# Kernel tuning notes

Measured on AMD Instinct MI355X. Metric: run time of the kernel, lower is better.

## Reference

```python
import jax, jax.numpy as jnp
import numpy as np

N_NODES = 200000
AVG_DEG = 64
N_EDGES = N_NODES * AVG_DEG
ALPHA = 0.1
DT = 0.01
EPS = 1e-9
DIFF = 10.0
HARD_LO = -jnp.pi / 2
HARD_HI = jnp.pi / 2


def setup_inputs() -> dict:
    key = jax.random.key(0)
    ks = jax.random.split(key, 8)
    xy = jax.random.normal(ks[0], (N_NODES, 2), dtype=jnp.float32)
    xy_dot_old = jax.random.normal(ks[1], (N_NODES, 2), dtype=jnp.float32)
    scale = 2.0 * np.pi
    phase = (jax.random.uniform(ks[2], (N_NODES,), dtype=jnp.float32) * 2 - 1) * scale
    w = (jax.random.uniform(ks[3], (N_NODES,), dtype=jnp.float32) * 2 - 1) * scale
    amplitudes = (jax.random.uniform(ks[4], (N_NODES,), dtype=jnp.float32) * 2 - 1) * scale
    ha = jax.random.normal(ks[5], (N_NODES,), dtype=jnp.float32)
    edge_src = jnp.sort(jax.random.randint(ks[6], (N_EDGES,), 0, N_NODES, dtype=jnp.int32))
    edge_dst = jax.random.randint(ks[7], (N_EDGES,), 0, N_NODES, dtype=jnp.int32)
    return {
        "xy": xy,
        "xy_dot_old": xy_dot_old,
        "phase": phase,
        "w": w,
        "amplitudes": amplitudes,
        "ha": ha,
        "edge_src": edge_src,
        "edge_dst": edge_dst,
    }


def reference(xy, xy_dot_old, phase, w, amplitudes, ha, edge_src, edge_dst):
    n = xy.shape[0]
    x, y = xy[:, 0], xy[:, 1]
    xd_old, yd_old = xy_dot_old[:, 0], xy_dot_old[:, 1]

    # per-node gain matrix K_i = [[a, -b], [b, a]]
    r2 = x * x + y * y
    a = ALPHA * (1.0 - r2 * r2)                         # term_a
    zeta = 1.0 - ha * ((xd_old + EPS) / (jnp.abs(xd_old) + EPS))
    b = w / (zeta + EPS)                                # term_b
    kx = a * x - b * y                                  # (K_i @ xy_i).x
    ky = b * x + a * y                                  # (K_i @ xy_i).y

    # edge coupling: R(phase_i - phase_j) @ xy_j, summed over neighbors j of i
    pd = phase[edge_src] - phase[edge_dst]
    c, s = jnp.cos(pd), jnp.sin(pd)
    xj = x[edge_dst]
    yj = y[edge_dst]
    ex = c * xj - s * yj
    ey = s * xj + c * yj
    sum_x = jax.ops.segment_sum(ex, edge_src, num_segments=n)
    sum_y = jax.ops.segment_sum(ey, edge_src, num_segments=n)

    # integrate with rate clamp
    x_dot = jnp.clip(kx + sum_x, xd_old - DIFF, xd_old + DIFF)
    y_dot = jnp.clip(ky + sum_y, yd_old - DIFF, yd_old + DIFF)
    x_new = x + x_dot * DT
    y_new = y + y_dot * DT

    angles = jnp.clip(amplitudes * y_new, HARD_LO, HARD_HI)
    xy_new = jnp.stack([x_new, y_new], axis=-1)
    xy_dot_old_new = xy  # original sets xy_dot_old[i] = old xy[i]
    return angles, xy_new, xy_dot_old_new
```

## Files before the change

kernel.cpp:

```cpp
#include <hip/hip_runtime.h>
#include <math.h>

#define ALPHA  0.1f
#define DT     0.01f
#define EPSV   1e-9f
#define DIFF   10.0f
#define HARD_P 1.5707963267948966f

__global__ void node_pre(const float2* __restrict__ xy,
                         const float*  __restrict__ phase,
                         float2* __restrict__ g,
                         float2* __restrict__ out_xyold,
                         float2* __restrict__ Gsum,
                         int n) {
    int i = blockIdx.x * blockDim.x + threadIdx.x;
    if (i >= n) return;
    float2 p = xy[i];
    float ph = phase[i];
    float s, c;
    sincosf(ph, &s, &c);
    float2 gv;
    gv.x = p.x * c + p.y * s;
    gv.y = p.y * c - p.x * s;
    g[i] = gv;
    out_xyold[i] = p;
    float2 z; z.x = 0.f; z.y = 0.f;
    Gsum[i] = z;
}

__global__ __launch_bounds__(256) void edge_seg(
        const int*    __restrict__ src,
        const int*    __restrict__ dst,
        const float2* __restrict__ g,
        float* __restrict__ Gsum,
        int n_edges) {
    const int e    = blockIdx.x * blockDim.x + threadIdx.x;
    const int lane = threadIdx.x & 63;
    const bool valid = (e < n_edges);

    int s = valid ? __builtin_nontemporal_load(src + e) : -1;
    int d = valid ? __builtin_nontemporal_load(dst + e) : 0;

    float ax = 0.f, ay = 0.f;
    if (valid) {
        float2 gd = g[d];
        ax = gd.x; ay = gd.y;
    }

    #pragma unroll
    for (int off = 1; off < 64; off <<= 1) {
        float px = __shfl_up(ax, off);
        float py = __shfl_up(ay, off);
        int   ps = __shfl_up(s,  off);
        if (lane >= off && ps == s) { ax += px; ay += py; }
    }

    int snext = __shfl_down(s, 1);
    bool tail = (lane == 63) || (snext != s);
    if (valid && tail) {
        atomicAdd(&Gsum[2*s],     ax);
        atomicAdd(&Gsum[2*s + 1], ay);
    }
}

__global__ void node_post(const float2* __restrict__ xy,
                          const float2* __restrict__ xyd,
                          const float*  __restrict__ phase,
                          const float*  __restrict__ w,
                          const float*  __restrict__ amps,
                          const float*  __restrict__ ha,
                          const float2* __restrict__ Gsum,
                          float* __restrict__ out,
                          int n) {
    int i = blockIdx.x * blockDim.x + threadIdx.x;
    if (i >= n) return;
    float2 p   = xy[i];
    float2 pdv = xyd[i];
    float x = p.x, y = p.y;
    float xd = pdv.x, yd = pdv.y;

    float r2 = x*x + y*y;
    float a = ALPHA * (1.0f - r2*r2);
    float h = ha[i];
    float zeta = 1.0f - h * ((xd + EPSV) / (fabsf(xd) + EPSV));
    float b = w[i] / (zeta + EPSV);
    float kx = a*x - b*y;
    float ky = b*x + a*y;

    float2 gv = Gsum[i];
    float s, c;
    sincosf(phase[i], &s, &c);
    float sumx = c*gv.x - s*gv.y;
    float sumy = s*gv.x + c*gv.y;

    float xdot = fminf(fmaxf(kx + sumx, xd - DIFF), xd + DIFF);
    float ydot = fminf(fmaxf(ky + sumy, yd - DIFF), yd + DIFF);
    float xn = x + xdot * DT;
    float yn = y + ydot * DT;

    float ang = fminf(fmaxf(amps[i] * yn, -HARD_P), HARD_P);

    out[i] = ang;
    float2* xy_new = (float2*)(out + n);
    float2 v; v.x = xn; v.y = yn;
    xy_new[i] = v;
}

extern "C" void kernel_launch(void* const* d_in, const int* in_sizes, int n_in,
                              void* d_out, int out_size, void* d_ws, size_t ws_size,
                              hipStream_t stream) {
    const float2* xy    = (const float2*)d_in[0];
    const float2* xyd   = (const float2*)d_in[1];
    const float*  phase = (const float*)d_in[2];
    const float*  w     = (const float*)d_in[3];
    const float*  amps  = (const float*)d_in[4];
    const float*  ha    = (const float*)d_in[5];
    const int*    esrc  = (const int*)d_in[6];
    const int*    edst  = (const int*)d_in[7];

    const int n       = in_sizes[2];
    const int n_edges = in_sizes[6];

    float* out = (float*)d_out;

    float2* g    = (float2*)d_ws;
    float2* Gsum = (float2*)((char*)d_ws + (size_t)n * sizeof(float2));

    const int B = 256;
    node_pre<<<(n + B - 1) / B, B, 0, stream>>>(
        xy, phase, g, (float2*)(out + (size_t)3 * n), Gsum, n);

    edge_seg<<<(n_edges + B - 1) / B, B, 0, stream>>>(
        esrc, edst, g, (float*)Gsum, n_edges);

    node_post<<<(n + B - 1) / B, B, 0, stream>>>(
        xy, xyd, phase, w, amps, ha, Gsum, out, n);
}
```

Measured before the change: 204.1 us.

## Process four edges per thread with vector loads and local segment reduction

The edge kernel now has each thread load four consecutive src/dst indices with 128-bit nontemporal loads and gather four g values. It reduces runs of equal source keys in registers before a wave-level segmented scan over 256 edges, so fewer threads, shuffles and atomics are needed per edge. In exchange the code is more complex: it handles the first and last segments of each thread separately, and the four-edge grouping may lower occupancy and memory-level parallelism.

```diff
diff --git a/kernel.cpp b/kernel.cpp
--- a/kernel.cpp
+++ b/kernel.cpp
@@ -1,11 +1,14 @@
 #include <hip/hip_runtime.h>
 #include <math.h>
+#include <limits.h>
 
 #define ALPHA  0.1f
 #define DT     0.01f
 #define EPSV   1e-9f
 #define DIFF   10.0f
 #define HARD_P 1.5707963267948966f
+
+typedef int v4i __attribute__((ext_vector_type(4)));
 
 __global__ void node_pre(const float2* __restrict__ xy,
                          const float*  __restrict__ phase,
@@ -28,38 +31,90 @@
     Gsum[i] = z;
 }
 
-__global__ __launch_bounds__(256) void edge_seg(
+__global__ __launch_bounds__(256) void edge_seg4(
         const int*    __restrict__ src,
         const int*    __restrict__ dst,
         const float2* __restrict__ g,
         float* __restrict__ Gsum,
         int n_edges) {
-    const int e    = blockIdx.x * blockDim.x + threadIdx.x;
     const int lane = threadIdx.x & 63;
-    const bool valid = (e < n_edges);
+    const int wib  = threadIdx.x >> 6;
+    const long wave = (long)blockIdx.x * 4 + wib;
+    const long base = wave * 256 + (long)lane * 4;
 
-    int s = valid ? __builtin_nontemporal_load(src + e) : -1;
-    int d = valid ? __builtin_nontemporal_load(dst + e) : 0;
+    int   sk[4];
+    float vx[4], vy[4];
 
-    float ax = 0.f, ay = 0.f;
-    if (valid) {
-        float2 gd = g[d];
-        ax = gd.x; ay = gd.y;
+    if (base + 3 < (long)n_edges) {
+        v4i sv = __builtin_nontemporal_load((const v4i*)(src + base));
+        v4i dv = __builtin_nontemporal_load((const v4i*)(dst + base));
+        sk[0]=sv.x; sk[1]=sv.y; sk[2]=sv.z; sk[3]=sv.w;
+        float2 g0 = g[dv.x];
+        float2 g1 = g[dv.y];
+        float2 g2 = g[dv.z];
+        float2 g3 = g[dv.w];
+        vx[0]=g0.x; vy[0]=g0.y; vx[1]=g1.x; vy[1]=g1.y;
+        vx[2]=g2.x; vy[2]=g2.y; vx[3]=g3.x; vy[3]=g3.y;
+    } else {
+        #pragma unroll
+        for (int j = 0; j < 4; ++j) {
+            long e = base + j;
+            if (e < (long)n_edges) {
+                sk[j] = src[e];
+                float2 gd = g[dst[e]];
+                vx[j] = gd.x; vy[j] = gd.y;
+            } else {
+                sk[j] = INT_MAX;
+                vx[j] = 0.f; vy[j] = 0.f;
+            }
+        }
     }
 
+    int   kF = sk[0], rk = sk[0];
+    float fx = 0.f, fy = 0.f;
+    float rx = vx[0], ry = vy[0];
+    bool  firstClosed = false;
+    #pragma unroll
+    for (int j = 1; j < 4; ++j) {
+        if (sk[j] == rk) {
+            rx += vx[j]; ry += vy[j];
+        } else {
+            if (!firstClosed) { fx = rx; fy = ry; firstClosed = true; }
+            else {
+                atomicAdd(&Gsum[2*rk],   rx);
+                atomicAdd(&Gsum[2*rk+1], ry);
+            }
+            rk = sk[j]; rx = vx[j]; ry = vy[j];
+        }
+    }
+    const int  kL   = rk;
+    const bool pure = !firstClosed;
+
+    float ax = rx, ay = ry;
+    int   key = kL;
     #pragma unroll
     for (int off = 1; off < 64; off <<= 1) {
         float px = __shfl_up(ax, off);
         float py = __shfl_up(ay, off);
-        int   ps = __shfl_up(s,  off);
-        if (lane >= off && ps == s) { ax += px; ay += py; }
+        int   pk = __shfl_up(key, off);
+        if (lane >= off && pk == key) { ax += px; ay += py; }
     }
 
-    int snext = __shfl_down(s, 1);
-    bool tail = (lane == 63) || (snext != s);
-    if (valid && tail) {
-        atomicAdd(&Gsum[2*s],     ax);
-        atomicAdd(&Gsum[2*s + 1], ay);
+    float pscx = __shfl_up(ax, 1);
+    float pscy = __shfl_up(ay, 1);
+    int   pKL  = __shfl_up(key, 1);
+    int   nKF  = __shfl_down(kF, 1);
+
+    if (!pure) {
+        float gx_ = fx, gy_ = fy;
+        if (lane > 0 && pKL == kF) { gx_ += pscx; gy_ += pscy; }
+        atomicAdd(&Gsum[2*kF],   gx_);
+        atomicAdd(&Gsum[2*kF+1], gy_);
+    }
+    bool endHere = (lane == 63) || (nKF != key);
+    if (key != INT_MAX && endHere) {
+        atomicAdd(&Gsum[2*key],   ax);
+        atomicAdd(&Gsum[2*key+1], ay);
     }
 }
 
@@ -130,8 +185,8 @@
     node_pre<<<(n + B - 1) / B, B, 0, stream>>>(
         xy, phase, g, (float2*)(out + (size_t)3 * n), Gsum, n);
 
-    edge_seg<<<(n_edges + B - 1) / B, B, 0, stream>>>(
-        esrc, edst, g, (float*)Gsum, n_edges);
+    int n_blocks = (n_edges + 1023) / 1024;
+    edge_seg4<<<n_blocks, B, 0, stream>>>(esrc, edst, g, (float*)Gsum, n_edges);
 
     node_post<<<(n + B - 1) / B, B, 0, stream>>>(
         xy, xyd, phase, w, amps, ha, Gsum, out, n);
```

After: 199.9 us. -2.0%, faster.
